# Performance work log

Measured on AMD Instinct MI355X. Metric: run time of the kernel, lower is better.

Reference implementation:

```python
import math
import jax, jax.numpy as jnp
import numpy as np

B, L, H, DH, DV = 4, 4096, 16, 128, 128
CHUNK = 1024
ROPE_BASE = 10000.0


def _rope_tables(length, dim, base, dtype):
    half = dim // 2
    freqs = jnp.exp(jnp.arange(half, dtype=jnp.float32) * (-(math.log(base) / half)))
    angles = jnp.arange(length, dtype=jnp.float32)[:, None] * freqs[None, :]  # (L, half)
    return jnp.cos(angles).astype(dtype), jnp.sin(angles).astype(dtype)


def _apply_rope(x, cos, sin):
    # x: (B, L, H, D); cos/sin: (L, D/2) -> broadcast (1, L, 1, D/2)
    half = x.shape[-1] // 2
    x1, x2 = x[..., :half], x[..., half:]
    c = cos[None, :, None, :]
    s = sin[None, :, None, :]
    return jnp.concatenate([x1 * c - x2 * s, x2 * c + x1 * s], axis=-1)


def setup_inputs() -> dict:
    key = jax.random.key(0)
    kq, kk, kv = jax.random.split(key, 3)
    q = jax.random.normal(kq, (B, L, H, DH), dtype=jnp.float32)
    k = jax.random.normal(kk, (B, L, H, DH), dtype=jnp.float32)
    v = jax.random.normal(kv, (B, L, H, DV), dtype=jnp.float32)
    return {"q": q, "k": k, "v": v}


def reference(q, k, v):
    b, l, h, dh = q.shape
    dv = v.shape[-1]
    n = l // CHUNK  # number of chunks

    cos, sin = _rope_tables(l, dh, ROPE_BASE, q.dtype)
    q = _apply_rope(q, cos, sin)
    k = _apply_rope(k, cos, sin)

    # Chunk-local causal attention: reshape to (B, N, H, C, D)
    qc = q.reshape(b, n, CHUNK, h, dh).transpose(0, 1, 3, 2, 4)
    kc = k.reshape(b, n, CHUNK, h, dh).transpose(0, 1, 3, 2, 4)
    vc = v.reshape(b, n, CHUNK, h, dv).transpose(0, 1, 3, 2, 4)

    scale = 1.0 / math.sqrt(dh)
    scores = jnp.einsum("bnhqd,bnhkd->bnhqk", qc, kc) * scale
    causal = jnp.tril(jnp.ones((CHUNK, CHUNK), dtype=bool))
    scores = jnp.where(causal[None, None, None], scores, jnp.finfo(scores.dtype).min)
    probs = jax.nn.softmax(scores, axis=-1)
    out = jnp.einsum("bnhqk,bnhkd->bnhqd", probs, vc)

    # back to (B, L, H, Dv)
    return out.transpose(0, 1, 3, 2, 4).reshape(b, l, h, dv)
```

## Files before the change

kernel.cpp:

```cpp
#include <hip/hip_runtime.h>
#include <math.h>
#include <stdint.h>


typedef __attribute__((ext_vector_type(8)))  short bf16x8;
typedef __attribute__((ext_vector_type(4)))  short bf16x4;
typedef __attribute__((ext_vector_type(16))) float f32x16;
typedef __attribute__((ext_vector_type(4)))  float f32x4;
typedef __attribute__((ext_vector_type(4)))  unsigned short us4;

__device__ __forceinline__ unsigned short f2bf(float x) {
  unsigned u = __float_as_uint(x);
  u += 0x7fff + ((u >> 16) & 1);
  return (unsigned short)(u >> 16);
}

__global__ __launch_bounds__(256) void rope_kernel(
    const float* __restrict__ q, const float* __restrict__ k,
    unsigned short* __restrict__ qws, unsigned short* __restrict__ kws)
{
  const int w    = threadIdx.x >> 6;
  const int lane = threadIdx.x & 63;
  const int r    = blockIdx.x * 4 + w;
  const int b    = r >> 16;
  const int rem  = r & 65535;
  const int l    = rem >> 4;
  const int h    = rem & 15;
  const float freq  = __builtin_amdgcn_exp2f((float)lane * -0.20762050593046014f);
  const float angle = (float)l * freq;
  float sn, cs;
  sincosf(angle, &sn, &cs);
  const size_t src = (size_t)r * 128 + lane;
  const int n = l >> 10, ck = l & 1023;
  const size_t dst = ((((size_t)b * 4 + n) * 16 + h) * 1024 + ck) * 128 + lane;
  const float QS = 0.12751741f;
  float x1 = q[src], x2 = q[src + 64];
  qws[dst]      = f2bf((x1 * cs - x2 * sn) * QS);
  qws[dst + 64] = f2bf((x2 * cs + x1 * sn) * QS);
  x1 = k[src]; x2 = k[src + 64];
  kws[dst]      = f2bf(x1 * cs - x2 * sn);
  kws[dst + 64] = f2bf(x2 * cs + x1 * sn);
}

__global__ __launch_bounds__(256) void vtrans_kernel(
    const float* __restrict__ v, unsigned short* __restrict__ vtws)
{
  __shared__ unsigned short tile[128 * 72];
  const int t   = threadIdx.x;
  const int ckb = blockIdx.x & 15;
  const int h   = (blockIdx.x >> 4) & 15;
  const int n   = (blockIdx.x >> 8) & 3;
  const int b   = blockIdx.x >> 10;
  const int i0  = (t >> 4) * 4;
  const int dv0 = (t & 15) * 8;
  const int l0  = n * 1024 + ckb * 64;
  const float* src = v + (((size_t)b * 4096 + l0) * 16 + h) * 128;
  unsigned short vals[4][8];
#pragma unroll
  for (int i = 0; i < 4; ++i) {
    const float* p = src + (size_t)(i0 + i) * 2048 + dv0;
    f32x4 a = *(const f32x4*)p;
    f32x4 c = *(const f32x4*)(p + 4);
#pragma unroll
    for (int jj = 0; jj < 4; ++jj) { vals[i][jj] = f2bf(a[jj]); vals[i][4 + jj] = f2bf(c[jj]); }
  }
#pragma unroll
  for (int dd = 0; dd < 8; ++dd) {
    us4 pk = { vals[0][dd], vals[1][dd], vals[2][dd], vals[3][dd] };
    *(us4*)&tile[(dv0 + dd) * 72 + i0] = pk;
  }
  __syncthreads();
  const int dv = t >> 1, hf = t & 1;
  const size_t dstb = ((((size_t)b * 4 + n) * 16 + h) * 128 + dv) * 1024 + ckb * 64 + hf * 32;
  const unsigned short* sl = &tile[dv * 72 + hf * 32];
#pragma unroll
  for (int kk = 0; kk < 4; ++kk)
    *(uint4*)(vtws + dstb + kk * 8) = *(const uint4*)(sl + kk * 8);
}

__global__ __launch_bounds__(256) void attn_kernel(
    const unsigned short* __restrict__ qws, const unsigned short* __restrict__ kws,
    const unsigned short* __restrict__ vtws, float* __restrict__ out)
{
  __shared__ unsigned short smem[64 * 136 + 128 * 72];
  unsigned short* kt = smem;
  unsigned short* vt = smem + 64 * 136;
  unsigned short* qstage = smem;

  const int qt   = blockIdx.x;
  const int nh   = blockIdx.y;
  const int b    = blockIdx.z;
  const int t    = threadIdx.x;
  const int lane = t & 63;
  const int w    = t >> 6;
  const int c    = lane & 31;
  const int g    = lane >> 5;

  const size_t bnh = (size_t)b * 64 + nh;
  const unsigned short* qbase = qws + bnh * (1024 * 128) + (size_t)qt * (128 * 128);
  const unsigned short* kbase = kws + bnh * (1024 * 128);
  const unsigned short* vbase = vtws + bnh * (128 * 1024);

#pragma unroll
  for (int it = 0; it < 8; ++it) {
    int u = it * 256 + t;
    int row = u >> 4, col = u & 15;
    uint4 val = ((const uint4*)qbase)[u];
    *(uint4*)((char*)qstage + row * 272 + col * 16) = val;
  }
  __syncthreads();
  const int qsub = w * 32;
  bf16x8 qf[8];
  {
    const char* qp = (const char*)qstage + (qsub + c) * 272 + g * 16;
#pragma unroll
    for (int f = 0; f < 8; ++f) qf[f] = *(const bf16x8*)(qp + f * 32);
  }
  __syncthreads();

  f32x16 acc[4] = {};
  float m_run = -INFINITY, l_run = 0.0f;
  const int q0w  = qt * 128 + qsub;
  const int rowq = q0w + c;
  const int jmax = 2 * qt + 2;

  for (int j = 0; j < jmax; ++j) {
    const uint4* kg = (const uint4*)(kbase + (size_t)j * (64 * 128));
#pragma unroll
    for (int it = 0; it < 4; ++it) {
      int u = it * 256 + t;
      int row = u >> 4, col = u & 15;
      uint4 val = kg[u];
      *(uint4*)((char*)kt + row * 272 + col * 16) = val;
    }
#pragma unroll
    for (int it = 0; it < 4; ++it) {
      int u = it * 256 + t;
      int dv = u >> 3, col = u & 7;
      uint4 val = *(const uint4*)(vbase + (size_t)dv * 1024 + j * 64 + col * 8);
      *(uint4*)((char*)vt + dv * 144 + col * 16) = val;
    }
    __syncthreads();

    const int kv0 = j * 64;
    if (kv0 <= q0w + 31) {
      f32x16 s[2];
#pragma unroll
      for (int ks = 0; ks < 2; ++ks) {
        f32x16 a = {};
        const char* kp = (const char*)kt + (ks * 32 + c) * 272 + g * 16;
#pragma unroll
        for (int f = 0; f < 8; ++f) {
          bf16x8 kf = *(const bf16x8*)(kp + f * 32);
          a = __builtin_amdgcn_mfma_f32_32x32x16_bf16(kf, qf[f], a, 0, 0, 0);
        }
        s[ks] = a;
      }
      const bool needmask = (kv0 + 63) > q0w;
      float mloc = -INFINITY;
      if (needmask) {
#pragma unroll
        for (int ks = 0; ks < 2; ++ks)
#pragma unroll
          for (int r = 0; r < 16; ++r) {
            int kv = kv0 + ks * 32 + (r & 3) + 8 * (r >> 2) + 4 * g;
            float val = (kv > rowq) ? -3.0e38f : s[ks][r];
            s[ks][r] = val;
            mloc = fmaxf(mloc, val);
          }
      } else {
#pragma unroll
        for (int ks = 0; ks < 2; ++ks)
#pragma unroll
          for (int r = 0; r < 16; ++r) mloc = fmaxf(mloc, s[ks][r]);
      }
      mloc = fmaxf(mloc, __shfl_xor(mloc, 32));
      const float mnew  = fmaxf(m_run, mloc);
      const float alpha = __builtin_amdgcn_exp2f(m_run - mnew);
      float rsum = 0.0f;
#pragma unroll
      for (int ks = 0; ks < 2; ++ks)
#pragma unroll
        for (int r = 0; r < 16; ++r) {
          float p = __builtin_amdgcn_exp2f(s[ks][r] - mnew);
          s[ks][r] = p;
          rsum += p;
        }
      rsum += __shfl_xor(rsum, 32);
      l_run = l_run * alpha + rsum;
      m_run = mnew;
#pragma unroll
      for (int d = 0; d < 4; ++d)
#pragma unroll
        for (int r = 0; r < 16; ++r) acc[d][r] *= alpha;
      bf16x4 pfr[8];
#pragma unroll
      for (int o = 0; o < 8; ++o) {
        const int ks = o >> 2, rb = 4 * (o & 3);
        unsigned u0 = __float_as_uint(s[ks][rb + 0]); u0 += 0x7fff + ((u0 >> 16) & 1);
        unsigned u1 = __float_as_uint(s[ks][rb + 1]); u1 += 0x7fff + ((u1 >> 16) & 1);
        unsigned u2 = __float_as_uint(s[ks][rb + 2]); u2 += 0x7fff + ((u2 >> 16) & 1);
        unsigned u3 = __float_as_uint(s[ks][rb + 3]); u3 += 0x7fff + ((u3 >> 16) & 1);
        union { unsigned uu[2]; bf16x4 bv; } pk;
        pk.uu[0] = __builtin_amdgcn_perm(u1, u0, 0x07060302u);
        pk.uu[1] = __builtin_amdgcn_perm(u3, u2, 0x07060302u);
        pfr[o] = pk.bv;
      }
      const char* vp = (const char*)vt + c * 144 + g * 8;
#pragma unroll
      for (int d = 0; d < 4; ++d) {
        f32x16 a = acc[d];
        const char* vpd = vp + d * 32 * 144;
#pragma unroll
        for (int o = 0; o < 8; ++o) {
          bf16x4 vf = *(const bf16x4*)(vpd + o * 16);
          a = __builtin_amdgcn_mfma_f32_32x32x8bf16_1k(vf, pfr[o], a, 0, 0, 0);
        }
        acc[d] = a;
      }
    }
    __syncthreads();
  }

  const float invl = 1.0f / l_run;
  const int n = nh >> 4, h = nh & 15;
  const size_t orow = (((size_t)b * 4096 + n * 1024 + rowq) * 16 + h) * 128;
#pragma unroll
  for (int d = 0; d < 4; ++d)
#pragma unroll
    for (int e = 0; e < 4; ++e) {
      f32x4 vv;
#pragma unroll
      for (int rr = 0; rr < 4; ++rr) vv[rr] = acc[d][4 * e + rr] * invl;
      *(f32x4*)(out + orow + 32 * d + 8 * e + 4 * g) = vv;
    }
}

extern "C" void kernel_launch(void* const* d_in, const int* in_sizes, int n_in,
                              void* d_out, int out_size, void* d_ws, size_t ws_size,
                              hipStream_t stream) {
  const float* q = (const float*)d_in[0];
  const float* k = (const float*)d_in[1];
  const float* v = (const float*)d_in[2];
  float* out = (float*)d_out;
  unsigned short* qws  = (unsigned short*)d_ws;
  unsigned short* kws  = qws + (size_t)33554432;
  unsigned short* vtws = kws + (size_t)33554432;

  rope_kernel<<<65536, 256, 0, stream>>>(q, k, qws, kws);
  vtrans_kernel<<<4096, 256, 0, stream>>>(v, vtws);
  attn_kernel<<<dim3(8, 64, 4), 256, 0, stream>>>(qws, kws, vtws, out);
}
```

Before: 610.0 us.

## Prefetch K/V into registers, precompute RoPE table, vectorize rope, reorder attention blocks

New measurement: 955.5 us. 1.57x slower.

```diff
diff --git a/kernel.cpp b/kernel.cpp
--- a/kernel.cpp
+++ b/kernel.cpp
@@ -15,31 +15,69 @@
   return (unsigned short)(u >> 16);
 }
 
-__global__ __launch_bounds__(256) void rope_kernel(
-    const float* __restrict__ q, const float* __restrict__ k,
-    unsigned short* __restrict__ qws, unsigned short* __restrict__ kws)
-{
-  const int w    = threadIdx.x >> 6;
-  const int lane = threadIdx.x & 63;
-  const int r    = blockIdx.x * 4 + w;
-  const int b    = r >> 16;
-  const int rem  = r & 65535;
-  const int l    = rem >> 4;
-  const int h    = rem & 15;
-  const float freq  = __builtin_amdgcn_exp2f((float)lane * -0.20762050593046014f);
+__device__ __forceinline__ unsigned pk2(float lo, float hi) {
+  unsigned u0 = __float_as_uint(lo); u0 += 0x7fff + ((u0 >> 16) & 1);
+  unsigned u1 = __float_as_uint(hi); u1 += 0x7fff + ((u1 >> 16) & 1);
+  return __builtin_amdgcn_perm(u1, u0, 0x07060302u);
+}
+
+__global__ __launch_bounds__(256) void rope_tab_kernel(float* __restrict__ tab) {
+  const int idx = blockIdx.x * 256 + threadIdx.x;
+  const int l = idx >> 6, d = idx & 63;
+  const float freq  = __builtin_amdgcn_exp2f((float)d * -0.20762050593046014f);
   const float angle = (float)l * freq;
   float sn, cs;
   sincosf(angle, &sn, &cs);
-  const size_t src = (size_t)r * 128 + lane;
+  *(float2*)(tab + (size_t)idx * 2) = make_float2(cs, sn);
+}
+
+__global__ __launch_bounds__(256) void rope_kernel(
+    const float* __restrict__ q, const float* __restrict__ k,
+    const float* __restrict__ tab,
+    unsigned short* __restrict__ qws, unsigned short* __restrict__ kws)
+{
+  const int t  = threadIdx.x;
+  const int r  = blockIdx.x * 16 + (t >> 4);
+  const int j4 = (t & 15) * 4;
+  const int b   = r >> 16;
+  const int rem = r & 65535;
+  const int l   = rem >> 4;
+  const int h   = rem & 15;
+
+  const f32x4* tb = (const f32x4*)(tab + (size_t)l * 128 + (size_t)j4 * 2);
+  const f32x4 t0 = tb[0], t1 = tb[1];
+  const f32x4 cs = { t0[0], t0[2], t1[0], t1[2] };
+  const f32x4 sn = { t0[1], t0[3], t1[1], t1[3] };
+
+  const size_t src = (size_t)r * 128 + j4;
   const int n = l >> 10, ck = l & 1023;
-  const size_t dst = ((((size_t)b * 4 + n) * 16 + h) * 1024 + ck) * 128 + lane;
+  const size_t dst = ((((size_t)b * 4 + n) * 16 + h) * 1024 + ck) * 128 + j4;
   const float QS = 0.12751741f;
-  float x1 = q[src], x2 = q[src + 64];
-  qws[dst]      = f2bf((x1 * cs - x2 * sn) * QS);
-  qws[dst + 64] = f2bf((x2 * cs + x1 * sn) * QS);
-  x1 = k[src]; x2 = k[src + 64];
-  kws[dst]      = f2bf(x1 * cs - x2 * sn);
-  kws[dst + 64] = f2bf(x2 * cs + x1 * sn);
+
+  {
+    f32x4 x1 = *(const f32x4*)(q + src);
+    f32x4 x2 = *(const f32x4*)(q + src + 64);
+    f32x4 y1, y2;
+#pragma unroll
+    for (int i = 0; i < 4; ++i) {
+      y1[i] = (x1[i] * cs[i] - x2[i] * sn[i]) * QS;
+      y2[i] = (x2[i] * cs[i] + x1[i] * sn[i]) * QS;
+    }
+    *(uint2*)(qws + dst)      = make_uint2(pk2(y1[0], y1[1]), pk2(y1[2], y1[3]));
+    *(uint2*)(qws + dst + 64) = make_uint2(pk2(y2[0], y2[1]), pk2(y2[2], y2[3]));
+  }
+  {
+    f32x4 x1 = *(const f32x4*)(k + src);
+    f32x4 x2 = *(const f32x4*)(k + src + 64);
+    f32x4 y1, y2;
+#pragma unroll
+    for (int i = 0; i < 4; ++i) {
+      y1[i] = x1[i] * cs[i] - x2[i] * sn[i];
+      y2[i] = x2[i] * cs[i] + x1[i] * sn[i];
+    }
+    *(uint2*)(kws + dst)      = make_uint2(pk2(y1[0], y1[1]), pk2(y1[2], y1[3]));
+    *(uint2*)(kws + dst + 64) = make_uint2(pk2(y2[0], y2[1]), pk2(y2[2], y2[3]));
+  }
 }
 
 __global__ __launch_bounds__(256) void vtrans_kernel(
@@ -87,7 +125,7 @@
   unsigned short* vt = smem + 64 * 136;
   unsigned short* qstage = smem;
 
-  const int qt   = blockIdx.x;
+  const int qt   = 7 - (int)blockIdx.x;
   const int nh   = blockIdx.y;
   const int b    = blockIdx.z;
   const int t    = threadIdx.x;
@@ -101,6 +139,9 @@
   const unsigned short* kbase = kws + bnh * (1024 * 128);
   const unsigned short* vbase = vtws + bnh * (128 * 1024);
 
+  const int jmax = 2 * qt + 2;
+  uint4 kreg[4], vreg[4];
+
 #pragma unroll
   for (int it = 0; it < 8; ++it) {
     int u = it * 256 + t;
@@ -108,6 +149,16 @@
     uint4 val = ((const uint4*)qbase)[u];
     *(uint4*)((char*)qstage + row * 272 + col * 16) = val;
   }
+  {
+    const uint4* kg = (const uint4*)kbase;
+#pragma unroll
+    for (int it = 0; it < 4; ++it) kreg[it] = kg[it * 256 + t];
+#pragma unroll
+    for (int it = 0; it < 4; ++it) {
+      int u = it * 256 + t; int dv = u >> 3, col = u & 7;
+      vreg[it] = *(const uint4*)(vbase + (size_t)dv * 1024 + col * 8);
+    }
+  }
   __syncthreads();
   const int qsub = w * 32;
   bf16x8 qf[8];
@@ -117,30 +168,35 @@
     for (int f = 0; f < 8; ++f) qf[f] = *(const bf16x8*)(qp + f * 32);
   }
   __syncthreads();
+#pragma unroll
+  for (int it = 0; it < 4; ++it) {
+    int u = it * 256 + t; int row = u >> 4, col = u & 15;
+    *(uint4*)((char*)kt + row * 272 + col * 16) = kreg[it];
+  }
+#pragma unroll
+  for (int it = 0; it < 4; ++it) {
+    int u = it * 256 + t; int dv = u >> 3, col = u & 7;
+    *(uint4*)((char*)vt + dv * 144 + col * 16) = vreg[it];
+  }
+  __syncthreads();
 
   f32x16 acc[4] = {};
   float m_run = -INFINITY, l_run = 0.0f;
   const int q0w  = qt * 128 + qsub;
   const int rowq = q0w + c;
-  const int jmax = 2 * qt + 2;
 
   for (int j = 0; j < jmax; ++j) {
-    const uint4* kg = (const uint4*)(kbase + (size_t)j * (64 * 128));
-#pragma unroll
-    for (int it = 0; it < 4; ++it) {
-      int u = it * 256 + t;
-      int row = u >> 4, col = u & 15;
-      uint4 val = kg[u];
-      *(uint4*)((char*)kt + row * 272 + col * 16) = val;
-    }
-#pragma unroll
-    for (int it = 0; it < 4; ++it) {
-      int u = it * 256 + t;
-      int dv = u >> 3, col = u & 7;
-      uint4 val = *(const uint4*)(vbase + (size_t)dv * 1024 + j * 64 + col * 8);
-      *(uint4*)((char*)vt + dv * 144 + col * 16) = val;
-    }
-    __syncthreads();
+    const bool more = (j + 1) < jmax;
+    if (more) {
+      const uint4* kg = (const uint4*)(kbase + (size_t)(j + 1) * (64 * 128));
+#pragma unroll
+      for (int it = 0; it < 4; ++it) kreg[it] = kg[it * 256 + t];
+#pragma unroll
+      for (int it = 0; it < 4; ++it) {
+        int u = it * 256 + t; int dv = u >> 3, col = u & 7;
+        vreg[it] = *(const uint4*)(vbase + (size_t)dv * 1024 + (j + 1) * 64 + col * 8);
+      }
+    }
 
     const int kv0 = j * 64;
     if (kv0 <= q0w + 31) {
@@ -157,53 +213,61 @@
         s[ks] = a;
       }
       const bool needmask = (kv0 + 63) > q0w;
-      float mloc = -INFINITY;
+      float m0 = -3.0e38f, m1 = m0, m2 = m0, m3 = m0;
       if (needmask) {
 #pragma unroll
         for (int ks = 0; ks < 2; ++ks)
 #pragma unroll
-          for (int r = 0; r < 16; ++r) {
-            int kv = kv0 + ks * 32 + (r & 3) + 8 * (r >> 2) + 4 * g;
-            float val = (kv > rowq) ? -3.0e38f : s[ks][r];
-            s[ks][r] = val;
-            mloc = fmaxf(mloc, val);
+          for (int r = 0; r < 16; r += 4) {
+            const int base = kv0 + ks * 32 + 8 * (r >> 2) + 4 * g;
+            float v0 = (base + 0 > rowq) ? -3.0e38f : s[ks][r + 0];
+            float v1 = (base + 1 > rowq) ? -3.0e38f : s[ks][r + 1];
+            float v2 = (base + 2 > rowq) ? -3.0e38f : s[ks][r + 2];
+            float v3 = (base + 3 > rowq) ? -3.0e38f : s[ks][r + 3];
+            s[ks][r + 0] = v0; s[ks][r + 1] = v1; s[ks][r + 2] = v2; s[ks][r + 3] = v3;
+            m0 = fmaxf(m0, v0); m1 = fmaxf(m1, v1); m2 = fmaxf(m2, v2); m3 = fmaxf(m3, v3);
           }
       } else {
 #pragma unroll
         for (int ks = 0; ks < 2; ++ks)
 #pragma unroll
-          for (int r = 0; r < 16; ++r) mloc = fmaxf(mloc, s[ks][r]);
-      }
+          for (int r = 0; r < 16; r += 4) {
+            m0 = fmaxf(m0, s[ks][r + 0]); m1 = fmaxf(m1, s[ks][r + 1]);
+            m2 = fmaxf(m2, s[ks][r + 2]); m3 = fmaxf(m3, s[ks][r + 3]);
+          }
+      }
+      float mloc = fmaxf(fmaxf(m0, m1), fmaxf(m2, m3));
       mloc = fmaxf(mloc, __shfl_xor(mloc, 32));
-      const float mnew  = fmaxf(m_run, mloc);
-      const float alpha = __builtin_amdgcn_exp2f(m_run - mnew);
-      float rsum = 0.0f;
+      if (__any(mloc > m_run)) {
+        const float mnew  = fmaxf(m_run, mloc);
+        const float alpha = __builtin_amdgcn_exp2f(m_run - mnew);
+        l_run *= alpha;
+#pragma unroll
+        for (int d = 0; d < 4; ++d)
+#pragma unroll
+          for (int r = 0; r < 16; ++r) acc[d][r] *= alpha;
+        m_run = mnew;
+      }
+      float r0 = 0.0f, r1 = 0.0f, r2 = 0.0f, r3 = 0.0f;
 #pragma unroll
       for (int ks = 0; ks < 2; ++ks)
 #pragma unroll
-        for (int r = 0; r < 16; ++r) {
-          float p = __builtin_amdgcn_exp2f(s[ks][r] - mnew);
-          s[ks][r] = p;
-          rsum += p;
+        for (int r = 0; r < 16; r += 4) {
+          float p0 = __builtin_amdgcn_exp2f(s[ks][r + 0] - m_run); s[ks][r + 0] = p0; r0 += p0;
+          float p1 = __builtin_amdgcn_exp2f(s[ks][r + 1] - m_run); s[ks][r + 1] = p1; r1 += p1;
+          float p2 = __builtin_amdgcn_exp2f(s[ks][r + 2] - m_run); s[ks][r + 2] = p2; r2 += p2;
+          float p3 = __builtin_amdgcn_exp2f(s[ks][r + 3] - m_run); s[ks][r + 3] = p3; r3 += p3;
         }
+      float rsum = (r0 + r1) + (r2 + r3);
       rsum += __shfl_xor(rsum, 32);
-      l_run = l_run * alpha + rsum;
-      m_run = mnew;
-#pragma unroll
-      for (int d = 0; d < 4; ++d)
-#pragma unroll
-        for (int r = 0; r < 16; ++r) acc[d][r] *= alpha;
+      l_run += rsum;
       bf16x4 pfr[8];
 #pragma unroll
       for (int o = 0; o < 8; ++o) {
         const int ks = o >> 2, rb = 4 * (o & 3);
-        unsigned u0 = __float_as_uint(s[ks][rb + 0]); u0 += 0x7fff + ((u0 >> 16) & 1);
-        unsigned u1 = __float_as_uint(s[ks][rb + 1]); u1 += 0x7fff + ((u1 >> 16) & 1);
-        unsigned u2 = __float_as_uint(s[ks][rb + 2]); u2 += 0x7fff + ((u2 >> 16) & 1);
-        unsigned u3 = __float_as_uint(s[ks][rb + 3]); u3 += 0x7fff + ((u3 >> 16) & 1);
         union { unsigned uu[2]; bf16x4 bv; } pk;
-        pk.uu[0] = __builtin_amdgcn_perm(u1, u0, 0x07060302u);
-        pk.uu[1] = __builtin_amdgcn_perm(u3, u2, 0x07060302u);
+        pk.uu[0] = pk2(s[ks][rb + 0], s[ks][rb + 1]);
+        pk.uu[1] = pk2(s[ks][rb + 2], s[ks][rb + 3]);
         pfr[o] = pk.bv;
       }
       const char* vp = (const char*)vt + c * 144 + g * 8;
@@ -220,6 +284,19 @@
       }
     }
     __syncthreads();
+    if (more) {
+#pragma unroll
+      for (int it = 0; it < 4; ++it) {
+        int u = it * 256 + t; int row = u >> 4, col = u & 15;
+        *(uint4*)((char*)kt + row * 272 + col * 16) = kreg[it];
+      }
+#pragma unroll
+      for (int it = 0; it < 4; ++it) {
+        int u = it * 256 + t; int dv = u >> 3, col = u & 7;
+        *(uint4*)((char*)vt + dv * 144 + col * 16) = vreg[it];
+      }
+      __syncthreads();
+    }
   }
 
   const float invl = 1.0f / l_run;
@@ -247,7 +324,9 @@
   unsigned short* kws  = qws + (size_t)33554432;
   unsigned short* vtws = kws + (size_t)33554432;
 
-  rope_kernel<<<65536, 256, 0, stream>>>(q, k, qws, kws);
+  float* tab = (float*)vtws;
+  rope_tab_kernel<<<1024, 256, 0, stream>>>(tab);
+  rope_kernel<<<16384, 256, 0, stream>>>(q, k, tab, qws, kws);
   vtrans_kernel<<<4096, 256, 0, stream>>>(v, vtws);
   attn_kernel<<<dim3(8, 64, 4), 256, 0, stream>>>(qws, kws, vtws, out);
 }
```
